# Kernel tuning notes

Measured on AMD Instinct MI355X. Metric: run time of the kernel, lower is better.

Reference implementation:

```python
import jax, jax.numpy as jnp
import numpy as np

DIM = 180
HEADS = 6
HEAD_DIM = DIM // HEADS
SCALE = HEAD_DIM ** (-0.5)
BW, N, K = 8192, 64, 16


def setup_inputs() -> dict:
    key = jax.random.key(0)
    ks = jax.random.split(key, 6)
    return {
        "x": jax.random.normal(ks[0], (BW, N, DIM), dtype=jnp.float32),
        "bpe_windows": jax.random.normal(ks[1], (BW, N, K), dtype=jnp.float32),
        "qkv_w": jax.random.normal(ks[2], (3 * DIM, DIM), dtype=jnp.float32) * 0.05,
        "qkv_b": jax.random.normal(ks[3], (3 * DIM,), dtype=jnp.float32) * 0.05,
        "proj_w": jax.random.normal(ks[4], (DIM, DIM), dtype=jnp.float32) * 0.05,
        "proj_b": jax.random.normal(ks[5], (DIM,), dtype=jnp.float32) * 0.05,
        "tau": jnp.ones((HEADS, 1, 1), dtype=jnp.float32),
    }


def reference(x, bpe_windows, qkv_w, qkv_b, proj_w, proj_b, tau):
    B_, n, C = x.shape
    # qkv projection -> (3, B_, H, N, hd)
    qkv = (x @ qkv_w.T + qkv_b).reshape(B_, n, 3, HEADS, HEAD_DIM)
    qkv = jnp.transpose(qkv, (2, 0, 3, 1, 4))
    q, k, v = qkv[0], qkv[1], qkv[2]
    q = q * SCALE
    attn = jnp.einsum("bhid,bhjd->bhij", q, k)  # (B_, H, N, N)
    # geodesic bias from BPE embeddings: d_B(i,j) = ||bpe_i - bpe_j||_2
    diff = bpe_windows[:, :, None, :] - bpe_windows[:, None, :, :]  # (B_, N, N, K)
    d_B = jnp.sqrt(jnp.sum(diff * diff, axis=-1))  # (B_, N, N)
    log_W_geo = -d_B[:, None, :, :] / jnp.clip(tau, 1e-6)[None]  # (B_, H, N, N)
    attn = jax.nn.softmax(attn + log_W_geo, axis=-1)
    out = jnp.einsum("bhij,bhjd->bhid", attn, v)  # (B_, H, N, hd)
    out = jnp.transpose(out, (0, 2, 1, 3)).reshape(B_, n, C)
    return out @ proj_w.T + proj_b
```

## Files before the change

kernel.cpp:

```cpp
#include <hip/hip_runtime.h>
#include <math.h>

typedef __attribute__((ext_vector_type(8))) short short8b;
typedef __attribute__((ext_vector_type(4))) float f32x4;
typedef __attribute__((ext_vector_type(4))) unsigned short ushort4b;
typedef __attribute__((ext_vector_type(2))) unsigned short ushort2b;

#define NWIN 8192
#define NT   1024
#define SCALE 0.18257418583505536f

#define XB_P  200
#define QK_P  392
#define VT_P  72
#define DB_P  66
#define SCR_P 80
#define OST_P 180

#define OFF_XB  0
#define OFF_QK  25600
#define OFF_VT  75776
#define OFF_DB  103424
#define OFF_SCR 120320
#define LDS_BYTES 161280
#define OFF_OST OFF_QK
#define OFF_BPE OFF_SCR

#define WQ_ROWS 544
#define WK 192

__device__ __forceinline__ unsigned short f2bf(float f) {
    union { float f; unsigned int u; } v; v.f = f;
    return (unsigned short)((v.u + 0x7FFFu + ((v.u >> 16) & 1u)) >> 16);
}

__global__ void prep_weights(const float* __restrict__ qkv_w,
                             const float* __restrict__ proj_w,
                             unsigned short* __restrict__ wq,
                             unsigned short* __restrict__ wp)
{
    const int i = blockIdx.x * 256 + threadIdx.x;
    if (i < WQ_ROWS * WK) {
        const int r = i / WK, c = i % WK;
        wq[i] = f2bf((r < 540 && c < 180) ? qkv_w[r * 180 + c] : 0.f);
    }
    const int j = i - WQ_ROWS * WK;
    if (j >= 0 && j < 192 * WK) {
        const int r = j / WK, c = j % WK;
        wp[j] = f2bf((r < 180 && c < 180) ? proj_w[r * 180 + c] : 0.f);
    }
}

__global__ void __launch_bounds__(NT, 4)
waga_mfma(const float* __restrict__ x,
          const float* __restrict__ bpe,
          const unsigned short* __restrict__ wq,
          const unsigned short* __restrict__ wp,
          const float* __restrict__ qkv_b,
          const float* __restrict__ proj_b,
          const float* __restrict__ tau,
          float* __restrict__ out)
{
    extern __shared__ char smem[];
    unsigned short* xb   = (unsigned short*)(smem + OFF_XB);
    unsigned short* qk   = (unsigned short*)(smem + OFF_QK);
    unsigned short* vT   = (unsigned short*)(smem + OFF_VT);
    float*          dBs  = (float*)(smem + OFF_DB);
    unsigned short* scr  = (unsigned short*)(smem + OFF_SCR);
    float*          bpes = (float*)(smem + OFF_BPE);
    unsigned short* att  = xb;
    float*          ostage = (float*)(smem + OFF_OST);

    const int b = blockIdx.x;
    const int t = threadIdx.x;
    const int w = t >> 6;
    const int l = t & 63;
    const int lr = l & 15;
    const int g  = l >> 4;

    if (t < 320) {
        const int n = t / 5, c = t % 5;
        ushort4b z = {0, 0, 0, 0};
        *reinterpret_cast<ushort4b*>(xb + n * XB_P + 180 + 4 * c) = z;
    }
    if (t < 768) {
        const int tok = t / 12, r = t % 12;
        const int col = (r >> 1) * 64 + (r & 1) * 32 + 30;
        ushort2b z2 = {0, 0};
        *reinterpret_cast<ushort2b*>(qk + tok * QK_P + col) = z2;
    }
    {
        const float* xw = x + (size_t)b * (64 * 180);
        for (int i = t; i < 64 * 45; i += NT) {
            const int n = i / 45, c4 = i % 45;
            const float4 v = *reinterpret_cast<const float4*>(xw + i * 4);
            ushort4b o;
            o[0] = f2bf(v.x); o[1] = f2bf(v.y); o[2] = f2bf(v.z); o[3] = f2bf(v.w);
            *reinterpret_cast<ushort4b*>(xb + n * XB_P + c4 * 4) = o;
        }
    }
    if (t < 256) {
        const float* bw = bpe + (size_t)b * (64 * 16);
        const int n = t >> 2, k4 = t & 3;
        const float4 v = *reinterpret_cast<const float4*>(bw + t * 4);
        *reinterpret_cast<float4*>(bpes + n * 20 + 4 * k4) = v;
    }
    __syncthreads();

    {
        const int ti = t >> 4, tj = t & 15;
        float acc[4] = {0.f, 0.f, 0.f, 0.f};
        #pragma unroll
        for (int k4 = 0; k4 < 4; ++k4) {
            const float4 a = *reinterpret_cast<const float4*>(bpes + ti * 20 + 4 * k4);
            #pragma unroll
            for (int e = 0; e < 4; ++e) {
                const float4 bb = *reinterpret_cast<const float4*>(bpes + (tj + 16 * e) * 20 + 4 * k4);
                float d;
                d = a.x - bb.x; acc[e] += d * d;
                d = a.y - bb.y; acc[e] += d * d;
                d = a.z - bb.z; acc[e] += d * d;
                d = a.w - bb.w; acc[e] += d * d;
            }
        }
        #pragma unroll
        for (int e = 0; e < 4; ++e)
            dBs[ti * DB_P + tj + 16 * e] = sqrtf(acc[e]);
    }

    {
        const int nt0 = w, nt1 = w + 16, nt2q = 32 + w;
        const bool has2 = (w < 2);
        const int m0 = nt0 * 16 + lr, m1 = nt1 * 16 + lr, m2 = nt2q * 16 + lr;
        f32x4 acc0[4], acc1[4], acc2[4];
        const float b0 = (m0 < 540) ? qkv_b[m0] : 0.f;
        const float b1 = (m1 < 540) ? qkv_b[m1] : 0.f;
        const float b2 = (has2 && m2 < 540) ? qkv_b[m2] : 0.f;
        #pragma unroll
        for (int mt = 0; mt < 4; ++mt) {
            #pragma unroll
            for (int i = 0; i < 4; ++i) { acc0[mt][i] = b0; acc1[mt][i] = b1; acc2[mt][i] = b2; }
        }
        for (int kk = 0; kk < 6; ++kk) {
            short8b af[4];
            #pragma unroll
            for (int mt = 0; mt < 4; ++mt)
                af[mt] = *reinterpret_cast<const short8b*>(xb + (mt * 16 + lr) * XB_P + kk * 32 + g * 8);
            const short8b bf0 = *reinterpret_cast<const short8b*>(wq + (size_t)m0 * WK + kk * 32 + g * 8);
            #pragma unroll
            for (int mt = 0; mt < 4; ++mt)
                acc0[mt] = __builtin_amdgcn_mfma_f32_16x16x32_bf16(af[mt], bf0, acc0[mt], 0, 0, 0);
            const short8b bf1 = *reinterpret_cast<const short8b*>(wq + (size_t)m1 * WK + kk * 32 + g * 8);
            #pragma unroll
            for (int mt = 0; mt < 4; ++mt)
                acc1[mt] = __builtin_amdgcn_mfma_f32_16x16x32_bf16(af[mt], bf1, acc1[mt], 0, 0, 0);
            if (has2) {
                const short8b bf2 = *reinterpret_cast<const short8b*>(wq + (size_t)m2 * WK + kk * 32 + g * 8);
                #pragma unroll
                for (int mt = 0; mt < 4; ++mt)
                    acc2[mt] = __builtin_amdgcn_mfma_f32_16x16x32_bf16(af[mt], bf2, acc2[mt], 0, 0, 0);
            }
        }
        auto epi = [&](int m, f32x4* acc) {
            if (m < 540) {
                const int which = m / 180, mm = m % 180, hh = mm / 30, dd = mm % 30;
                #pragma unroll
                for (int mt = 0; mt < 4; ++mt)
                    #pragma unroll
                    for (int i = 0; i < 4; ++i) {
                        const int tok = mt * 16 + g * 4 + i;
                        const float v = acc[mt][i];
                        if (which == 0)      qk[tok * QK_P + hh * 64 + dd] = f2bf(v * SCALE);
                        else if (which == 1) qk[tok * QK_P + hh * 64 + 32 + dd] = f2bf(v);
                        else                 vT[hh * 2304 + dd * VT_P + tok] = f2bf(v);
                    }
            }
        };
        epi(m0, acc0);
        epi(m1, acc1);
        if (has2) epi(m2, acc2);
    }
    __syncthreads();

    {
        unsigned short* myscr = scr + w * (16 * SCR_P);
        for (int u = w; u < 24; u += 16) {
            const int h = u >> 2, mt = u & 3;
            const float it = 1.f / fmaxf(tau[h], 1e-6f);
            f32x4 s[4];
            #pragma unroll
            for (int nt2 = 0; nt2 < 4; ++nt2)
                #pragma unroll
                for (int i = 0; i < 4; ++i)
                    s[nt2][i] = -dBs[(mt * 16 + g * 4 + i) * DB_P + nt2 * 16 + lr] * it;
            const short8b qa = *reinterpret_cast<const short8b*>(qk + (mt * 16 + lr) * QK_P + h * 64 + g * 8);
            #pragma unroll
            for (int nt2 = 0; nt2 < 4; ++nt2) {
                const short8b kb = *reinterpret_cast<const short8b*>(qk + (nt2 * 16 + lr) * QK_P + h * 64 + 32 + g * 8);
                s[nt2] = __builtin_amdgcn_mfma_f32_16x16x32_bf16(qa, kb, s[nt2], 0, 0, 0);
            }
            float mx[4], sm[4];
            #pragma unroll
            for (int i = 0; i < 4; ++i)
                mx[i] = fmaxf(fmaxf(s[0][i], s[1][i]), fmaxf(s[2][i], s[3][i]));
            #pragma unroll
            for (int o = 1; o < 16; o <<= 1)
                #pragma unroll
                for (int i = 0; i < 4; ++i)
                    mx[i] = fmaxf(mx[i], __shfl_xor(mx[i], o, 16));
            #pragma unroll
            for (int i = 0; i < 4; ++i) sm[i] = 0.f;
            #pragma unroll
            for (int nt2 = 0; nt2 < 4; ++nt2)
                #pragma unroll
                for (int i = 0; i < 4; ++i) {
                    const float p = __expf(s[nt2][i] - mx[i]);
                    s[nt2][i] = p; sm[i] += p;
                }
            #pragma unroll
            for (int o = 1; o < 16; o <<= 1)
                #pragma unroll
                for (int i = 0; i < 4; ++i)
                    sm[i] += __shfl_xor(sm[i], o, 16);
            #pragma unroll
            for (int i = 0; i < 4; ++i) sm[i] = 1.f / sm[i];
            #pragma unroll
            for (int nt2 = 0; nt2 < 4; ++nt2)
                #pragma unroll
                for (int i = 0; i < 4; ++i)
                    myscr[(g * 4 + i) * SCR_P + nt2 * 16 + lr] = f2bf(s[nt2][i] * sm[i]);
            f32x4 o0 = {0.f, 0.f, 0.f, 0.f}, o1 = {0.f, 0.f, 0.f, 0.f};
            #pragma unroll
            for (int ks = 0; ks < 2; ++ks) {
                const short8b pa = *reinterpret_cast<const short8b*>(myscr + lr * SCR_P + ks * 32 + g * 8);
                const short8b v0 = *reinterpret_cast<const short8b*>(vT + h * 2304 + lr * VT_P + ks * 32 + g * 8);
                const short8b v1 = *reinterpret_cast<const short8b*>(vT + h * 2304 + (16 + lr) * VT_P + ks * 32 + g * 8);
                o0 = __builtin_amdgcn_mfma_f32_16x16x32_bf16(pa, v0, o0, 0, 0, 0);
                o1 = __builtin_amdgcn_mfma_f32_16x16x32_bf16(pa, v1, o1, 0, 0, 0);
            }
            #pragma unroll
            for (int i = 0; i < 4; ++i) {
                const int tok = mt * 16 + g * 4 + i;
                att[tok * XB_P + h * 30 + lr] = f2bf(o0[i]);
                if (lr < 14)
                    att[tok * XB_P + h * 30 + 16 + lr] = f2bf(o1[i]);
            }
        }
    }
    __syncthreads();

    {
        for (int tid = 3 * w; tid < 3 * w + 3; ++tid) {
            const int nt = tid >> 2, mt = tid & 3;
            f32x4 acc = {0.f, 0.f, 0.f, 0.f};
            for (int kk = 0; kk < 6; ++kk) {
                const short8b af = *reinterpret_cast<const short8b*>(att + (mt * 16 + lr) * XB_P + kk * 32 + g * 8);
                const short8b bf = *reinterpret_cast<const short8b*>(wp + (nt * 16 + lr) * WK + kk * 32 + g * 8);
                acc = __builtin_amdgcn_mfma_f32_16x16x32_bf16(af, bf, acc, 0, 0, 0);
            }
            const int mcol = nt * 16 + lr;
            if (mcol < 180) {
                const float pb = proj_b[mcol];
                #pragma unroll
                for (int i = 0; i < 4; ++i)
                    ostage[(mt * 16 + g * 4 + i) * OST_P + mcol] = acc[i] + pb;
            }
        }
    }
    __syncthreads();

    {
        const float4* src = (const float4*)ostage;
        float4* dst = (float4*)(out + (size_t)b * (64 * 180));
        for (int i = t; i < 64 * 180 / 4; i += NT) dst[i] = src[i];
    }
}

extern "C" void kernel_launch(void* const* d_in, const int* in_sizes, int n_in,
                              void* d_out, int out_size, void* d_ws, size_t ws_size,
                              hipStream_t stream) {
    (void)in_sizes; (void)n_in; (void)out_size; (void)ws_size;
    const float* x      = (const float*)d_in[0];
    const float* bpe    = (const float*)d_in[1];
    const float* qkv_w  = (const float*)d_in[2];
    const float* qkv_b  = (const float*)d_in[3];
    const float* proj_w = (const float*)d_in[4];
    const float* proj_b = (const float*)d_in[5];
    const float* tau    = (const float*)d_in[6];

    unsigned short* wq = (unsigned short*)d_ws;
    unsigned short* wp = wq + WQ_ROWS * WK;

    prep_weights<<<(WQ_ROWS * WK + 192 * WK + 255) / 256, 256, 0, stream>>>(qkv_w, proj_w, wq, wp);

    (void)hipFuncSetAttribute((const void*)waga_mfma,
                              hipFuncAttributeMaxDynamicSharedMemorySize,
                              LDS_BYTES);
    waga_mfma<<<NWIN, NT, LDS_BYTES, stream>>>(x, bpe, wq, wp, qkv_b, proj_b, tau,
                                               (float*)d_out);
}
```

Measured before the change: 775.5 us.

## Split QKV and attention into two head-group passes to shrink LDS footprint

QKV projection and attention are processed in two passes of three heads each, with weights reordered per pass, so the LDS needed drops from about 160KB to about 79KB, allowing two blocks per CU. The geodesic distance matrix is stored as fp16. Attention output is staged in the block's own slice of the global output buffer instead of LDS. The projection result is written straight to global memory without an LDS staging copy. This trades an extra barrier pass, uncoalesced output stores and global round-trips of the attention tile for higher occupancy.

```diff
diff --git a/kernel.cpp b/kernel.cpp
--- a/kernel.cpp
+++ b/kernel.cpp
@@ -1,4 +1,5 @@
 #include <hip/hip_runtime.h>
+#include <hip/hip_fp16.h>
 #include <math.h>
 
 typedef __attribute__((ext_vector_type(8))) short short8b;
@@ -10,24 +11,19 @@
 #define NT   1024
 #define SCALE 0.18257418583505536f
 
-#define XB_P  200
-#define QK_P  392
-#define VT_P  72
-#define DB_P  66
-#define SCR_P 80
-#define OST_P 180
-
+#define XB_P 200
+#define QK_P 200
+#define VT_P 72
+#define DB_P 68
 #define OFF_XB  0
 #define OFF_QK  25600
-#define OFF_VT  75776
-#define OFF_DB  103424
-#define OFF_SCR 120320
-#define LDS_BYTES 161280
-#define OFF_OST OFF_QK
-#define OFF_BPE OFF_SCR
-
-#define WQ_ROWS 544
+#define OFF_VT  51200
+#define OFF_DB  65024
+#define OFF_BPE 73728
+#define LDS_BYTES 78848
+
 #define WK 192
+#define ATT_P 184
 
 __device__ __forceinline__ unsigned short f2bf(float f) {
     union { float f; unsigned int u; } v; v.f = f;
@@ -36,25 +32,29 @@
 
 __global__ void prep_weights(const float* __restrict__ qkv_w,
                              const float* __restrict__ proj_w,
-                             unsigned short* __restrict__ wq,
+                             unsigned short* __restrict__ wq2,
                              unsigned short* __restrict__ wp)
 {
-    const int i = blockIdx.x * 256 + threadIdx.x;
-    if (i < WQ_ROWS * WK) {
-        const int r = i / WK, c = i % WK;
-        wq[i] = f2bf((r < 540 && c < 180) ? qkv_w[r * 180 + c] : 0.f);
-    }
-    const int j = i - WQ_ROWS * WK;
-    if (j >= 0 && j < 192 * WK) {
+    const int idx = blockIdx.x * 256 + threadIdx.x;
+    if (idx < 2 * 270 * WK) {
+        const int p = idx / (270 * WK);
+        const int rr = (idx / WK) % 270;
+        const int kcol = idx % WK;
+        const int which = rr / 90, hh = (rr % 90) / 30, dd = rr % 30;
+        const int r_orig = which * 180 + (3 * p + hh) * 30 + dd;
+        wq2[idx] = f2bf((kcol < 180) ? qkv_w[r_orig * 180 + kcol] : 0.f);
+    }
+    const int j = idx - 2 * 270 * WK;
+    if (j >= 0 && j < WK * WK) {
         const int r = j / WK, c = j % WK;
         wp[j] = f2bf((r < 180 && c < 180) ? proj_w[r * 180 + c] : 0.f);
     }
 }
 
-__global__ void __launch_bounds__(NT, 4)
+__global__ void __launch_bounds__(NT, 8)
 waga_mfma(const float* __restrict__ x,
           const float* __restrict__ bpe,
-          const unsigned short* __restrict__ wq,
+          const unsigned short* __restrict__ wq2,
           const unsigned short* __restrict__ wp,
           const float* __restrict__ qkv_b,
           const float* __restrict__ proj_b,
@@ -63,13 +63,10 @@
 {
     extern __shared__ char smem[];
     unsigned short* xb   = (unsigned short*)(smem + OFF_XB);
-    unsigned short* qk   = (unsigned short*)(smem + OFF_QK);
-    unsigned short* vT   = (unsigned short*)(smem + OFF_VT);
-    float*          dBs  = (float*)(smem + OFF_DB);
-    unsigned short* scr  = (unsigned short*)(smem + OFF_SCR);
+    unsigned short* qk3  = (unsigned short*)(smem + OFF_QK);
+    unsigned short* vT3  = (unsigned short*)(smem + OFF_VT);
+    unsigned short* dBs  = (unsigned short*)(smem + OFF_DB);
     float*          bpes = (float*)(smem + OFF_BPE);
-    unsigned short* att  = xb;
-    float*          ostage = (float*)(smem + OFF_OST);
 
     const int b = blockIdx.x;
     const int t = threadIdx.x;
@@ -78,19 +75,25 @@
     const int lr = l & 15;
     const int g  = l >> 4;
 
-    if (t < 320) {
-        const int n = t / 5, c = t % 5;
+    unsigned short* attg = (unsigned short*)((char*)out + (size_t)b * 46080 + 22528);
+
+    if (t < 192) {
+        const int n = t / 3, c = t % 3;
         ushort4b z = {0, 0, 0, 0};
         *reinterpret_cast<ushort4b*>(xb + n * XB_P + 180 + 4 * c) = z;
-    }
-    if (t < 768) {
-        const int tok = t / 12, r = t % 12;
+    } else if (t < 576) {
+        const int i = t - 192;
+        const int n = i / 6, r = i % 6;
         const int col = (r >> 1) * 64 + (r & 1) * 32 + 30;
         ushort2b z2 = {0, 0};
-        *reinterpret_cast<ushort2b*>(qk + tok * QK_P + col) = z2;
+        *reinterpret_cast<ushort2b*>(qk3 + n * QK_P + col) = z2;
+    } else if (t < 640) {
+        const int n = t - 576;
+        ushort4b z = {0, 0, 0, 0};
+        *reinterpret_cast<ushort4b*>(attg + n * ATT_P + 180) = z;
     }
     {
-        const float* xw = x + (size_t)b * (64 * 180);
+        const float* xw = x + (size_t)b * 11520;
         for (int i = t; i < 64 * 45; i += NT) {
             const int n = i / 45, c4 = i % 45;
             const float4 v = *reinterpret_cast<const float4*>(xw + i * 4);
@@ -100,10 +103,8 @@
         }
     }
     if (t < 256) {
-        const float* bw = bpe + (size_t)b * (64 * 16);
-        const int n = t >> 2, k4 = t & 3;
-        const float4 v = *reinterpret_cast<const float4*>(bw + t * 4);
-        *reinterpret_cast<float4*>(bpes + n * 20 + 4 * k4) = v;
+        const float4 v = *reinterpret_cast<const float4*>(bpe + (size_t)b * 1024 + t * 4);
+        *reinterpret_cast<float4*>(bpes + (t >> 2) * 20 + (t & 3) * 4) = v;
     }
     __syncthreads();
 
@@ -125,154 +126,180 @@
         }
         #pragma unroll
         for (int e = 0; e < 4; ++e)
-            dBs[ti * DB_P + tj + 16 * e] = sqrtf(acc[e]);
-    }
-
-    {
-        const int nt0 = w, nt1 = w + 16, nt2q = 32 + w;
-        const bool has2 = (w < 2);
-        const int m0 = nt0 * 16 + lr, m1 = nt1 * 16 + lr, m2 = nt2q * 16 + lr;
-        f32x4 acc0[4], acc1[4], acc2[4];
-        const float b0 = (m0 < 540) ? qkv_b[m0] : 0.f;
-        const float b1 = (m1 < 540) ? qkv_b[m1] : 0.f;
-        const float b2 = (has2 && m2 < 540) ? qkv_b[m2] : 0.f;
+            dBs[ti * DB_P + tj + 16 * e] =
+                __half_as_ushort(__float2half_rn(sqrtf(acc[e])));
+    }
+
+    for (int pass = 0; pass < 2; ++pass) {
+        if (pass) __syncthreads();
+
+        const unsigned short* wqp = wq2 + (size_t)pass * 270 * WK;
+        for (int tile = w; tile < 18; tile += 16) {
+            const int seg = tile >> 1;
+            const int which = seg / 3, hh = seg % 3;
+            const int wbase = which * 90 + hh * 30;
+            const int ddr = ((tile & 1) << 4) + lr;
+            const bool arow_ok = (ddr < 30);
+            const int ddb = ((tile & 1) << 4) + (g << 2);
+            const int bbase = which * 180 + (3 * pass + hh) * 30 + ddb;
+            float bias[4];
+            #pragma unroll
+            for (int i = 0; i < 4; ++i)
+                bias[i] = (ddb + i < 30) ? qkv_b[bbase + i] : 0.f;
+            f32x4 acc[4];
+            #pragma unroll
+            for (int mt = 0; mt < 4; ++mt) {
+                acc[mt][0] = bias[0]; acc[mt][1] = bias[1];
+                acc[mt][2] = bias[2]; acc[mt][3] = bias[3];
+            }
+            #pragma unroll
+            for (int kk = 0; kk < 6; ++kk) {
+                short8b af;
+                if (arow_ok)
+                    af = *reinterpret_cast<const short8b*>(
+                        wqp + (size_t)(wbase + ddr) * WK + kk * 32 + g * 8);
+                else
+                    af = short8b{0,0,0,0,0,0,0,0};
+                #pragma unroll
+                for (int mt = 0; mt < 4; ++mt) {
+                    const short8b bf = *reinterpret_cast<const short8b*>(
+                        xb + (mt * 16 + lr) * XB_P + kk * 32 + g * 8);
+                    acc[mt] = __builtin_amdgcn_mfma_f32_16x16x32_bf16(af, bf, acc[mt], 0, 0, 0);
+                }
+            }
+            #pragma unroll
+            for (int mt = 0; mt < 4; ++mt) {
+                const int tok = mt * 16 + lr;
+                float v0 = acc[mt][0], v1 = acc[mt][1], v2 = acc[mt][2], v3 = acc[mt][3];
+                if (which == 0) { v0 *= SCALE; v1 *= SCALE; v2 *= SCALE; v3 *= SCALE; }
+                if (which < 2) {
+                    unsigned short* dst = qk3 + tok * QK_P + hh * 64 + which * 32 + ddb;
+                    if (ddb < 28) {
+                        ushort4b o = { f2bf(v0), f2bf(v1), f2bf(v2), f2bf(v3) };
+                        *reinterpret_cast<ushort4b*>(dst) = o;
+                    } else {
+                        ushort2b o = { f2bf(v0), f2bf(v1) };
+                        *reinterpret_cast<ushort2b*>(dst) = o;
+                    }
+                } else {
+                    const int c = (tok & 32) + ((tok >> 2) & 3) * 8 + ((tok >> 4) & 1) * 4 + (tok & 3);
+                    unsigned short* base = vT3 + hh * 2304 + c;
+                    if (ddb + 0 < 30) base[(ddb + 0) * VT_P] = f2bf(v0);
+                    if (ddb + 1 < 30) base[(ddb + 1) * VT_P] = f2bf(v1);
+                    if (ddb + 2 < 30) base[(ddb + 2) * VT_P] = f2bf(v2);
+                    if (ddb + 3 < 30) base[(ddb + 3) * VT_P] = f2bf(v3);
+                }
+            }
+        }
+        __syncthreads();
+
+        if (w < 12) {
+            const int hh = w >> 2, mt = w & 3;
+            const int h = 3 * pass + hh;
+            const float itau = 1.f / fmaxf(tau[h], 1e-6f);
+            f32x4 s[4];
+            #pragma unroll
+            for (int jt = 0; jt < 4; ++jt)
+                #pragma unroll
+                for (int i = 0; i < 4; ++i) {
+                    const float d = __half2float(__ushort_as_half(
+                        dBs[(jt * 16 + g * 4 + i) * DB_P + mt * 16 + lr]));
+                    s[jt][i] = -d * itau;
+                }
+            const short8b qf = *reinterpret_cast<const short8b*>(
+                qk3 + (mt * 16 + lr) * QK_P + hh * 64 + g * 8);
+            #pragma unroll
+            for (int jt = 0; jt < 4; ++jt) {
+                const short8b kf = *reinterpret_cast<const short8b*>(
+                    qk3 + (jt * 16 + lr) * QK_P + hh * 64 + 32 + g * 8);
+                s[jt] = __builtin_amdgcn_mfma_f32_16x16x32_bf16(kf, qf, s[jt], 0, 0, 0);
+            }
+            float mx = s[0][0];
+            #pragma unroll
+            for (int jt = 0; jt < 4; ++jt)
+                #pragma unroll
+                for (int i = 0; i < 4; ++i) mx = fmaxf(mx, s[jt][i]);
+            mx = fmaxf(mx, __shfl_xor(mx, 16));
+            mx = fmaxf(mx, __shfl_xor(mx, 32));
+            float sum = 0.f;
+            #pragma unroll
+            for (int jt = 0; jt < 4; ++jt)
+                #pragma unroll
+                for (int i = 0; i < 4; ++i) {
+                    const float p = __expf(s[jt][i] - mx);
+                    s[jt][i] = p; sum += p;
+                }
+            sum += __shfl_xor(sum, 16);
+            sum += __shfl_xor(sum, 32);
+            const float inv = 1.f / sum;
+            short8b pb[2];
+            #pragma unroll
+            for (int ks = 0; ks < 2; ++ks) {
+                pb[ks][0] = (short)f2bf(s[2 * ks][0] * inv);
+                pb[ks][1] = (short)f2bf(s[2 * ks][1] * inv);
+                pb[ks][2] = (short)f2bf(s[2 * ks][2] * inv);
+                pb[ks][3] = (short)f2bf(s[2 * ks][3] * inv);
+                pb[ks][4] = (short)f2bf(s[2 * ks + 1][0] * inv);
+                pb[ks][5] = (short)f2bf(s[2 * ks + 1][1] * inv);
+                pb[ks][6] = (short)f2bf(s[2 * ks + 1][2] * inv);
+                pb[ks][7] = (short)f2bf(s[2 * ks + 1][3] * inv);
+            }
+            const int tok = mt * 16 + lr;
+            #pragma unroll
+            for (int ntd = 0; ntd < 2; ++ntd) {
+                f32x4 o = {0.f, 0.f, 0.f, 0.f};
+                #pragma unroll
+                for (int ks = 0; ks < 2; ++ks) {
+                    const short8b va = *reinterpret_cast<const short8b*>(
+                        vT3 + hh * 2304 + (ntd * 16 + lr) * VT_P + ks * 32 + g * 8);
+                    o = __builtin_amdgcn_mfma_f32_16x16x32_bf16(va, pb[ks], o, 0, 0, 0);
+                }
+                const int col = h * 30 + ntd * 16 + g * 4;
+                unsigned short* dst = attg + tok * ATT_P + col;
+                if (ntd == 0 || g < 3) {
+                    ushort4b ov = { f2bf(o[0]), f2bf(o[1]), f2bf(o[2]), f2bf(o[3]) };
+                    *reinterpret_cast<ushort4b*>(dst) = ov;
+                } else {
+                    ushort2b ov = { f2bf(o[0]), f2bf(o[1]) };
+                    *reinterpret_cast<ushort2b*>(dst) = ov;
+                }
+            }
+        }
+    }
+    __syncthreads();
+
+    f32x4 pacc[3];
+    #pragma unroll
+    for (int q3 = 0; q3 < 3; ++q3) {
+        const int tid = 3 * w + q3;
+        const int nt = tid >> 2, mt = tid & 3;
+        f32x4 acc = {0.f, 0.f, 0.f, 0.f};
         #pragma unroll
-        for (int mt = 0; mt < 4; ++mt) {
-            #pragma unroll
-            for (int i = 0; i < 4; ++i) { acc0[mt][i] = b0; acc1[mt][i] = b1; acc2[mt][i] = b2; }
-        }
         for (int kk = 0; kk < 6; ++kk) {
-            short8b af[4];
-            #pragma unroll
-            for (int mt = 0; mt < 4; ++mt)
-                af[mt] = *reinterpret_cast<const short8b*>(xb + (mt * 16 + lr) * XB_P + kk * 32 + g * 8);
-            const short8b bf0 = *reinterpret_cast<const short8b*>(wq + (size_t)m0 * WK + kk * 32 + g * 8);
-            #pragma unroll
-            for (int mt = 0; mt < 4; ++mt)
-                acc0[mt] = __builtin_amdgcn_mfma_f32_16x16x32_bf16(af[mt], bf0, acc0[mt], 0, 0, 0);
-            const short8b bf1 = *reinterpret_cast<const short8b*>(wq + (size_t)m1 * WK + kk * 32 + g * 8);
-            #pragma unroll
-            for (int mt = 0; mt < 4; ++mt)
-                acc1[mt] = __builtin_amdgcn_mfma_f32_16x16x32_bf16(af[mt], bf1, acc1[mt], 0, 0, 0);
-            if (has2) {
-                const short8b bf2 = *reinterpret_cast<const short8b*>(wq + (size_t)m2 * WK + kk * 32 + g * 8);
-                #pragma unroll
-                for (int mt = 0; mt < 4; ++mt)
-                    acc2[mt] = __builtin_amdgcn_mfma_f32_16x16x32_bf16(af[mt], bf2, acc2[mt], 0, 0, 0);
-            }
-        }
-        auto epi = [&](int m, f32x4* acc) {
-            if (m < 540) {
-                const int which = m / 180, mm = m % 180, hh = mm / 30, dd = mm % 30;
-                #pragma unroll
-                for (int mt = 0; mt < 4; ++mt)
-                    #pragma unroll
-                    for (int i = 0; i < 4; ++i) {
-                        const int tok = mt * 16 + g * 4 + i;
-                        const float v = acc[mt][i];
-                        if (which == 0)      qk[tok * QK_P + hh * 64 + dd] = f2bf(v * SCALE);
-                        else if (which == 1) qk[tok * QK_P + hh * 64 + 32 + dd] = f2bf(v);
-                        else                 vT[hh * 2304 + dd * VT_P + tok] = f2bf(v);
-                    }
-            }
-        };
-        epi(m0, acc0);
-        epi(m1, acc1);
-        if (has2) epi(m2, acc2);
+            short8b af;
+            if (kk == 5 && g == 3)
+                af = short8b{0,0,0,0,0,0,0,0};
+            else
+                af = *reinterpret_cast<const short8b*>(
+                    attg + (mt * 16 + lr) * ATT_P + kk * 32 + g * 8);
+            const short8b bf = *reinterpret_cast<const short8b*>(
+                wp + (nt * 16 + lr) * WK + kk * 32 + g * 8);
+            acc = __builtin_amdgcn_mfma_f32_16x16x32_bf16(af, bf, acc, 0, 0, 0);
+        }
+        pacc[q3] = acc;
     }
     __syncthreads();
-
-    {
-        unsigned short* myscr = scr + w * (16 * SCR_P);
-        for (int u = w; u < 24; u += 16) {
-            const int h = u >> 2, mt = u & 3;
-            const float it = 1.f / fmaxf(tau[h], 1e-6f);
-            f32x4 s[4];
-            #pragma unroll
-            for (int nt2 = 0; nt2 < 4; ++nt2)
-                #pragma unroll
-                for (int i = 0; i < 4; ++i)
-                    s[nt2][i] = -dBs[(mt * 16 + g * 4 + i) * DB_P + nt2 * 16 + lr] * it;
-            const short8b qa = *reinterpret_cast<const short8b*>(qk + (mt * 16 + lr) * QK_P + h * 64 + g * 8);
-            #pragma unroll
-            for (int nt2 = 0; nt2 < 4; ++nt2) {
-                const short8b kb = *reinterpret_cast<const short8b*>(qk + (nt2 * 16 + lr) * QK_P + h * 64 + 32 + g * 8);
-                s[nt2] = __builtin_amdgcn_mfma_f32_16x16x32_bf16(qa, kb, s[nt2], 0, 0, 0);
-            }
-            float mx[4], sm[4];
+    #pragma unroll
+    for (int q3 = 0; q3 < 3; ++q3) {
+        const int tid = 3 * w + q3;
+        const int nt = tid >> 2, mt = tid & 3;
+        const int chan = nt * 16 + lr;
+        if (chan < 180) {
+            const float pbv = proj_b[chan];
             #pragma unroll
             for (int i = 0; i < 4; ++i)
-                mx[i] = fmaxf(fmaxf(s[0][i], s[1][i]), fmaxf(s[2][i], s[3][i]));
-            #pragma unroll
-            for (int o = 1; o < 16; o <<= 1)
-                #pragma unroll
-                for (int i = 0; i < 4; ++i)
-                    mx[i] = fmaxf(mx[i], __shfl_xor(mx[i], o, 16));
-            #pragma unroll
-            for (int i = 0; i < 4; ++i) sm[i] = 0.f;
-            #pragma unroll
-            for (int nt2 = 0; nt2 < 4; ++nt2)
-                #pragma unroll
-                for (int i = 0; i < 4; ++i) {
-                    const float p = __expf(s[nt2][i] - mx[i]);
-                    s[nt2][i] = p; sm[i] += p;
-                }
-            #pragma unroll
-            for (int o = 1; o < 16; o <<= 1)
-                #pragma unroll
-                for (int i = 0; i < 4; ++i)
-                    sm[i] += __shfl_xor(sm[i], o, 16);
-            #pragma unroll
-            for (int i = 0; i < 4; ++i) sm[i] = 1.f / sm[i];
-            #pragma unroll
-            for (int nt2 = 0; nt2 < 4; ++nt2)
-                #pragma unroll
-                for (int i = 0; i < 4; ++i)
-                    myscr[(g * 4 + i) * SCR_P + nt2 * 16 + lr] = f2bf(s[nt2][i] * sm[i]);
-            f32x4 o0 = {0.f, 0.f, 0.f, 0.f}, o1 = {0.f, 0.f, 0.f, 0.f};
-            #pragma unroll
-            for (int ks = 0; ks < 2; ++ks) {
-                const short8b pa = *reinterpret_cast<const short8b*>(myscr + lr * SCR_P + ks * 32 + g * 8);
-                const short8b v0 = *reinterpret_cast<const short8b*>(vT + h * 2304 + lr * VT_P + ks * 32 + g * 8);
-                const short8b v1 = *reinterpret_cast<const short8b*>(vT + h * 2304 + (16 + lr) * VT_P + ks * 32 + g * 8);
-                o0 = __builtin_amdgcn_mfma_f32_16x16x32_bf16(pa, v0, o0, 0, 0, 0);
-                o1 = __builtin_amdgcn_mfma_f32_16x16x32_bf16(pa, v1, o1, 0, 0, 0);
-            }
-            #pragma unroll
-            for (int i = 0; i < 4; ++i) {
-                const int tok = mt * 16 + g * 4 + i;
-                att[tok * XB_P + h * 30 + lr] = f2bf(o0[i]);
-                if (lr < 14)
-                    att[tok * XB_P + h * 30 + 16 + lr] = f2bf(o1[i]);
-            }
-        }
-    }
-    __syncthreads();
-
-    {
-        for (int tid = 3 * w; tid < 3 * w + 3; ++tid) {
-            const int nt = tid >> 2, mt = tid & 3;
-            f32x4 acc = {0.f, 0.f, 0.f, 0.f};
-            for (int kk = 0; kk < 6; ++kk) {
-                const short8b af = *reinterpret_cast<const short8b*>(att + (mt * 16 + lr) * XB_P + kk * 32 + g * 8);
-                const short8b bf = *reinterpret_cast<const short8b*>(wp + (nt * 16 + lr) * WK + kk * 32 + g * 8);
-                acc = __builtin_amdgcn_mfma_f32_16x16x32_bf16(af, bf, acc, 0, 0, 0);
-            }
-            const int mcol = nt * 16 + lr;
-            if (mcol < 180) {
-                const float pb = proj_b[mcol];
-                #pragma unroll
-                for (int i = 0; i < 4; ++i)
-                    ostage[(mt * 16 + g * 4 + i) * OST_P + mcol] = acc[i] + pb;
-            }
-        }
-    }
-    __syncthreads();
-
-    {
-        const float4* src = (const float4*)ostage;
-        float4* dst = (float4*)(out + (size_t)b * (64 * 180));
-        for (int i = t; i < 64 * 180 / 4; i += NT) dst[i] = src[i];
+                out[((size_t)b * 64 + mt * 16 + g * 4 + i) * 180 + chan] = pacc[q3][i] + pbv;
+        }
     }
 }
 
@@ -288,14 +315,15 @@
     const float* proj_b = (const float*)d_in[5];
     const float* tau    = (const float*)d_in[6];
 
-    unsigned short* wq = (unsigned short*)d_ws;
-    unsigned short* wp = wq + WQ_ROWS * WK;
-
-    prep_weights<<<(WQ_ROWS * WK + 192 * WK + 255) / 256, 256, 0, stream>>>(qkv_w, proj_w, wq, wp);
+    unsigned short* wq2 = (unsigned short*)d_ws;
+    unsigned short* wp  = wq2 + 2 * 270 * WK;
+
+    prep_weights<<<(2 * 270 * WK + WK * WK + 255) / 256, 256, 0, stream>>>(
+        qkv_w, proj_w, wq2, wp);
 
     (void)hipFuncSetAttribute((const void*)waga_mfma,
                               hipFuncAttributeMaxDynamicSharedMemorySize,
                               LDS_BYTES);
-    waga_mfma<<<NWIN, NT, LDS_BYTES, stream>>>(x, bpe, wq, wp, qkv_b, proj_b, tau,
+    waga_mfma<<<NWIN, NT, LDS_BYTES, stream>>>(x, bpe, wq2, wp, qkv_b, proj_b, tau,
                                                (float*)d_out);
 }
```

After: 799.7 us. 1.03x slower.
